# Kernel tuning notes

Hardware: AMD Instinct MI355X
Metric: run time of the kernel (lower is better)

Reference implementation:

```python
import jax, jax.numpy as jnp
import numpy as np

B, L, C, H, W = 4, 16, 64, 64, 64
F, NH, NB = 128, 2, 2


def _ln(x, w, b, eps=1e-5):
    # LayerNorm over last two dims (H, W), torch-style biased variance
    m = jnp.mean(x, axis=(-2, -1), keepdims=True)
    v = jnp.var(x, axis=(-2, -1), keepdims=True)
    return (x - m) * jax.lax.rsqrt(v + eps) * w + b


def _conv2d(x, w, b):
    # x: (N, Cin, H, W), w: (Cout, Cin, k, k) -- the (1,k,k) Conv3d acts per-frame
    y = jax.lax.conv_general_dilated(x, w, (1, 1), 'SAME',
                                     dimension_numbers=('NCHW', 'OIHW', 'NCHW'))
    return y + b[None, :, None, None]


def _combine(c1, c2):
    a1, b1 = c1
    a2, b2 = c2
    return a1 * a2, a2 * b1 + b2


def _forward(x, params_log, pBw_r, pBw_i, pBb_r, pBb_i, pCw_r, pCw_i, pCb_r, pCb_i,
             lru_ln_w, lru_ln_b, cin_w, cin_b, h3_w, h3_b, h1_w, h1_b,
             h_ln_w, h_ln_b, cout_w, cout_b, ffn_ln_w, ffn_ln_b):
    gelu = lambda t: jax.nn.gelu(t, approximate=False)
    Bsz, Ln, Cc, Hh, Ww = x.shape
    for i in range(NB):
        # ---- ConvLRULayer ----
        pl = params_log[i]
        nu = jnp.exp(pl[:Cc])            # (C, H)
        theta = jnp.exp(pl[Cc:2 * Cc])   # (C, H)
        gamma = jnp.exp(pl[2 * Cc:])     # (C, H)
        lamb = jnp.exp(jax.lax.complex(-nu, theta))  # (C, H) complex
        Bw = jax.lax.complex(pBw_r[i], pBw_i[i])
        Bb = jax.lax.complex(pBb_r[i], pBb_i[i])
        Cw = jax.lax.complex(pCw_r[i], pCw_i[i])
        Cb = jax.lax.complex(pCb_r[i], pCb_i[i])
        h = jnp.fft.fft2(x.astype(jnp.complex64), axes=(-2, -1))  # (B,L,C,H,W)
        h = jnp.einsum('blchw,oc->blohw', h, Bw) + Bb[None, None, :, None, None]
        h = h * gamma[None, None, :, :, None]
        # parallel scan: h[t] = lamb * h[t-1] + h[t] along L
        a = jnp.broadcast_to(lamb[None, None, :, :, None], (Bsz, Ln, Cc, Hh, 1))
        _, h = jax.lax.associative_scan(_combine, (a, h), axis=1)
        h = jnp.fft.ifft2(h, axes=(-2, -1))
        h = jnp.einsum('blchw,oc->blohw', h, Cw) + Cb[None, None, :, None, None]
        h = _ln(h.real, lru_ln_w[i], lru_ln_b[i])
        x = h + x
        # ---- FeedForward (all Conv3d have kernel 1 in L -> per-frame 2D) ----
        y = x.reshape(Bsz * Ln, Cc, Hh, Ww)
        y_ = gelu(_conv2d(y, cin_w[i], cin_b[i]))  # (B*L, F, H, W)
        for j in range(NH):
            t = gelu(_conv2d(y_, h3_w[i, j], h3_b[i, j]))
            t = gelu(jnp.einsum('nfhw,of->nohw', t, h1_w[i, j])
                     + h1_b[i, j][None, :, None, None])
            y_ = _ln(t, h_ln_w[i, j], h_ln_b[i, j]) + y_
        t = jnp.einsum('nfhw,of->nohw', y_, cout_w[i]) + cout_b[i][None, :, None, None]
        t = _ln(t, ffn_ln_w[i], ffn_ln_b[i])
        x = t.reshape(Bsz, Ln, Cc, Hh, Ww) + x
    return x


def setup_inputs() -> dict:
    key = jax.random.key(0)
    ks = jax.random.split(key, 16)
    x = jax.random.normal(ks[0], (B, L, C, H, W), jnp.float32)
    # LRU stability init (as in the torch module)
    r_min, r_max = 0.8, 0.99
    u1 = jax.random.uniform(ks[1], (NB, C, H), jnp.float32)
    u2 = jax.random.uniform(ks[2], (NB, C, H), jnp.float32)
    nu_log = jnp.log(-0.5 * jnp.log(u1 * (r_max ** 2 - r_min ** 2) + r_min ** 2))
    theta_log = jnp.log(u2 * 2.0 * np.pi)
    gamma_log = 0.5 * jnp.log(1.0 - jnp.exp(-2.0 * jnp.exp(nu_log)))
    params_log = jnp.concatenate([nu_log, theta_log, gamma_log], axis=1)  # (NB, 3C, H)

    def nrm(k, shape, fan_in):
        return jax.random.normal(k, shape, jnp.float32) / np.sqrt(fan_in)

    return dict(
        x=x, params_log=params_log,
        pBw_r=nrm(ks[3], (NB, C, C), C), pBw_i=jnp.zeros((NB, C, C), jnp.float32),
        pBb_r=jnp.zeros((NB, C), jnp.float32), pBb_i=jnp.zeros((NB, C), jnp.float32),
        pCw_r=nrm(ks[4], (NB, C, C), C), pCw_i=jnp.zeros((NB, C, C), jnp.float32),
        pCb_r=jnp.zeros((NB, C), jnp.float32), pCb_i=jnp.zeros((NB, C), jnp.float32),
        lru_ln_w=jnp.ones((NB, H, W), jnp.float32), lru_ln_b=jnp.zeros((NB, H, W), jnp.float32),
        cin_w=nrm(ks[5], (NB, F, C, 7, 7), C * 49), cin_b=jnp.zeros((NB, F), jnp.float32),
        h3_w=nrm(ks[6], (NB, NH, F, F, 3, 3), F * 9), h3_b=jnp.zeros((NB, NH, F), jnp.float32),
        h1_w=nrm(ks[7], (NB, NH, F, F), F), h1_b=jnp.zeros((NB, NH, F), jnp.float32),
        h_ln_w=jnp.ones((NB, NH, H, W), jnp.float32), h_ln_b=jnp.zeros((NB, NH, H, W), jnp.float32),
        cout_w=nrm(ks[8], (NB, C, F), F), cout_b=jnp.zeros((NB, C), jnp.float32),
        ffn_ln_w=jnp.ones((NB, H, W), jnp.float32), ffn_ln_b=jnp.zeros((NB, H, W), jnp.float32),
    )


def reference(x, params_log, pBw_r, pBw_i, pBb_r, pBb_i, pCw_r, pCw_i, pCb_r, pCb_i,
              lru_ln_w, lru_ln_b, cin_w, cin_b, h3_w, h3_b, h1_w, h1_b,
              h_ln_w, h_ln_b, cout_w, cout_b, ffn_ln_w, ffn_ln_b):
    return _forward(x, params_log, pBw_r, pBw_i, pBb_r, pBb_i, pCw_r, pCw_i,
                    pCb_r, pCb_i, lru_ln_w, lru_ln_b, cin_w, cin_b, h3_w, h3_b,
                    h1_w, h1_b, h_ln_w, h_ln_b, cout_w, cout_b, ffn_ln_w, ffn_ln_b)
```

## Files before the change

kernel.cpp:

```cpp
#include <hip/hip_runtime.h>
#include <math.h>

static constexpr int Bd = 4, Ld = 16, Cd = 64, Hd = 64, Wd = 64, Fd = 128;
static constexpr int NBLK = 2, NHEAD = 2;
static constexpr int HW = 4096;
static constexpr float TWO_PI = 6.28318530717958647692f;

typedef __attribute__((ext_vector_type(8))) short bf16x8;
typedef __attribute__((ext_vector_type(4))) float f32x4;
typedef __attribute__((ext_vector_type(4))) unsigned int u32x4;

__device__ __forceinline__ float gelu_f(float v) {
    return 0.5f * v * (1.f + erff(v * 0.7071067811865476f));
}

__device__ __forceinline__ unsigned short bf16c(float f) {
    unsigned int u = __float_as_uint(f);
    unsigned int r = (u + 0x7fffu + ((u >> 16) & 1u)) >> 16;
    return (unsigned short)r;
}
__device__ __forceinline__ float bf2f(unsigned short u) {
    return __uint_as_float((unsigned int)u << 16);
}
__device__ __forceinline__ unsigned int packbf(float r, float i) {
    return (unsigned int)bf16c(r) | ((unsigned int)bf16c(i) << 16);
}
__device__ __forceinline__ bf16x8 bneg(bf16x8 v) {
    u32x4 u = *(u32x4*)&v;
    u = u ^ 0x80008000u;
    return *(bf16x8*)&u;
}

__device__ __forceinline__ void gl2lds16(const void* g, void* l) {
    __builtin_amdgcn_global_load_lds(
        (const __attribute__((address_space(1))) void*)g,
        (__attribute__((address_space(3))) void*)l, 16, 0, 0);
}

__global__ void k_prepdft(unsigned short* __restrict__ o) {
    int idx = blockIdx.x * 256 + threadIdx.x;
    if (idx >= 16384) return;
    int sec = idx >> 12, j = idx & 4095;
    int a = j >> 6, b = j & 63;
    float ang = (TWO_PI / 64.f) * (float)((a * b) & 63);
    float sv, cv;
    __sincosf(ang, &sv, &cv);
    float v;
    if (sec == 0) v = cv;
    else if (sec == 1) v = -sv;
    else if (sec == 2) v = cv * (1.f / 64.f);
    else v = -sv * (1.f / 64.f);
    o[idx] = bf16c(v);
}

__global__ void k_preplru(const float* __restrict__ bwr, const float* __restrict__ bwi,
                          const float* __restrict__ cwr, const float* __restrict__ cwi,
                          const float* __restrict__ gl,
                          unsigned short* __restrict__ wout, float* __restrict__ gamT) {
    int idx = blockIdx.x * 256 + threadIdx.x;
    if (idx < 16384) {
        int sec = idx >> 12, j = idx & 4095;
        const float* s = (sec == 0) ? bwr : (sec == 1) ? bwi : (sec == 2) ? cwr : cwi;
        wout[idx] = bf16c(s[j]);
    } else if (idx < 20480) {
        int j = idx - 16384;
        int fh = j >> 6, o2 = j & 63;
        gamT[j] = __expf(gl[o2 * 64 + fh]);
    }
}

__global__ __launch_bounds__(256) void k_dfthm(const float* __restrict__ x,
                                               unsigned int* __restrict__ X,
                                               const unsigned short* __restrict__ tcb,
                                               const unsigned short* __restrict__ tsb) {
    __shared__ __align__(16) unsigned char smm[49152];
    unsigned char* xpT = smm;
    unsigned char* tC = smm + 32768;
    unsigned char* tS = smm + 40960;
    int blk = blockIdx.x;
    int fi = blk >> 4;
    int w0 = (blk & 15) * 4;
    int t = threadIdx.x, lane = t & 63, wv = t >> 6;
    int pl = lane & 15, kg = lane >> 4;
    int l3 = lane >> 3, l7 = lane & 7;

    for (int q = 0; q < 2; ++q) {
        int sg = q * 4 + wv;
        gl2lds16(tcb + (size_t)(sg * 8 + l3) * 64 + (l7 ^ l3) * 8, tC + sg * 1024);
        gl2lds16(tsb + (size_t)(sg * 8 + l3) * 64 + (l7 ^ l3) * 8, tS + sg * 1024);
    }
    const float* xf = x + (size_t)fi * Cd * HW;
    int h = t & 63;
    for (int k = 0; k < 16; ++k) {
        int c = k * 4 + (t >> 6);
        float4 v = *(const float4*)(xf + (size_t)c * HW + h * 64 + w0);
        float vv[4] = {v.x, v.y, v.z, v.w};
#pragma unroll
        for (int q = 0; q < 4; ++q) {
            int pos = q * 64 + c;
            *(unsigned short*)(xpT + pos * 128 + ((h * 2) ^ ((c & 7) << 4))) = bf16c(vv[q]);
        }
    }
    __syncthreads();

    int w = w0 + wv;
    unsigned int* Xw = X + (size_t)fi * 262144 + (size_t)w * 4096;
    for (int half = 0; half < 2; ++half) {
        f32x4 aR[2][4], aI[2][4];
#pragma unroll
        for (int mt = 0; mt < 2; ++mt)
#pragma unroll
            for (int nt = 0; nt < 4; ++nt) { aR[mt][nt] = (f32x4)0.f; aI[mt][nt] = (f32x4)0.f; }
#pragma unroll
        for (int ks = 0; ks < 2; ++ks) {
            int koff = (ks * 64 + kg * 16);
            bf16x8 ac[2], as_[2], b[4];
#pragma unroll
            for (int mt = 0; mt < 2; ++mt) {
                int row = half * 32 + mt * 16 + pl;
                int off = row * 128 + (koff ^ ((pl & 7) << 4));
                ac[mt] = *(const bf16x8*)(tC + off);
                as_[mt] = *(const bf16x8*)(tS + off);
            }
#pragma unroll
            for (int nt = 0; nt < 4; ++nt) {
                int pos = wv * 64 + nt * 16 + pl;
                b[nt] = *(const bf16x8*)(xpT + pos * 128 + (koff ^ ((pl & 7) << 4)));
            }
#pragma unroll
            for (int mt = 0; mt < 2; ++mt)
#pragma unroll
                for (int nt = 0; nt < 4; ++nt) {
                    aR[mt][nt] = __builtin_amdgcn_mfma_f32_16x16x32_bf16(ac[mt], b[nt], aR[mt][nt], 0, 0, 0);
                    aI[mt][nt] = __builtin_amdgcn_mfma_f32_16x16x32_bf16(as_[mt], b[nt], aI[mt][nt], 0, 0, 0);
                }
        }
#pragma unroll
        for (int mt = 0; mt < 2; ++mt)
#pragma unroll
            for (int nt = 0; nt < 4; ++nt) {
                int c = nt * 16 + pl;
#pragma unroll
                for (int r = 0; r < 4; ++r) {
                    int fh = half * 32 + mt * 16 + kg * 4 + r;
                    Xw[fh * 64 + c] = packbf(aR[mt][nt][r], aI[mt][nt][r]);
                }
            }
    }
}

__global__ __launch_bounds__(256) void k_lrumid(unsigned int* __restrict__ X,
                                                const unsigned short* __restrict__ wbr,
                                                const unsigned short* __restrict__ wbi,
                                                const unsigned short* __restrict__ wcr,
                                                const unsigned short* __restrict__ wci,
                                                const float* __restrict__ gamT,
                                                const float* __restrict__ br_g,
                                                const float* __restrict__ bi_g,
                                                const float* __restrict__ plg) {
    __shared__ __align__(16) unsigned char smm[81920];
    unsigned char* inr = smm;
    unsigned char* ini = smm + 8192;
    unsigned char* hre = smm + 16384;
    unsigned char* him = smm + 24576;
    unsigned char* wBR = smm + 32768;
    unsigned char* wBI = smm + 40960;
    unsigned char* wCR = smm + 49152;
    unsigned char* wCI = smm + 57344;
    float* gam = (float*)(smm + 65536);
    int blk = blockIdx.x;
    int b = blk >> 6, s = blk & 63;
    int t = threadIdx.x, lane = t & 63, wv = t >> 6;
    int pj = lane & 15, kg = lane >> 4;
    int l3 = lane >> 3, l7 = lane & 7;

    for (int q = 0; q < 2; ++q) {
        int sg = q * 4 + wv;
        size_t goff = (size_t)(sg * 8 + l3) * 64 + (l7 ^ l3) * 8;
        gl2lds16(wbr + goff, wBR + sg * 1024);
        gl2lds16(wbi + goff, wBI + sg * 1024);
        gl2lds16(wcr + goff, wCR + sg * 1024);
        gl2lds16(wci + goff, wCI + sg * 1024);
    }
    for (int j = t; j < 4096; j += 256) gam[j] = gamT[j];

    float lamr[4][4], lami[4][4];
#pragma unroll
    for (int nt = 0; nt < 4; ++nt) {
        int o = nt * 16 + pj;
#pragma unroll
        for (int r = 0; r < 4; ++r) {
            int fh = wv * 16 + kg * 4 + r;
            float nu = expf(plg[o * 64 + fh]);
            float th = expf(plg[4096 + o * 64 + fh]);
            float mag = expf(-nu);
            float sth, cth;
            sincosf(th, &sth, &cth);
            lamr[nt][r] = mag * cth;
            lami[nt][r] = mag * sth;
        }
    }
    float bRo[4], bIo[4];
#pragma unroll
    for (int nt = 0; nt < 4; ++nt) {
        bRo[nt] = (s == 0) ? br_g[nt * 16 + pj] : 0.f;
        bIo[nt] = (s == 0) ? bi_g[nt * 16 + pj] : 0.f;
    }
    float str[4][4], sti[4][4];
    unsigned int* Xfrm = X + (size_t)b * 16 * 262144 + (size_t)s * 4096;

    for (int l = 0; l < 16; ++l) {
        unsigned int* Xi = Xfrm + (size_t)l * 262144;
        __syncthreads();
        for (int k = 0; k < 4; ++k) {
            int j = k * 256 + t;
            int row = j >> 4, c0 = (j & 15) * 4;
            u32x4 v = *(const u32x4*)(Xi + (size_t)row * 64 + c0);
            unsigned int rw0 = (v.x & 0xffffu) | (v.y << 16);
            unsigned int rw1 = (v.z & 0xffffu) | (v.w << 16);
            unsigned int iw0 = (v.x >> 16) | (v.y & 0xffff0000u);
            unsigned int iw1 = (v.z >> 16) | (v.w & 0xffff0000u);
            int off = row * 128 + ((((c0 >> 3) ^ (row & 7)) << 4) | ((c0 & 7) * 2));
            *(unsigned int*)(inr + off) = rw0;
            *(unsigned int*)(inr + off + 4) = rw1;
            *(unsigned int*)(ini + off) = iw0;
            *(unsigned int*)(ini + off + 4) = iw1;
        }
        __syncthreads();

        f32x4 cR[4], cI[4];
#pragma unroll
        for (int nt = 0; nt < 4; ++nt) { cR[nt] = (f32x4)0.f; cI[nt] = (f32x4)0.f; }
#pragma unroll
        for (int ks = 0; ks < 2; ++ks) {
            int koff = ks * 64 + kg * 16;
            int aoff = (wv * 16 + pj) * 128 + (koff ^ ((pj & 7) << 4));
            bf16x8 ar = *(const bf16x8*)(inr + aoff);
            bf16x8 ai = *(const bf16x8*)(ini + aoff);
            bf16x8 an = bneg(ai);
#pragma unroll
            for (int nt = 0; nt < 4; ++nt) {
                int o = nt * 16 + pj;
                int woff = o * 128 + (koff ^ ((pj & 7) << 4));
                bf16x8 brf = *(const bf16x8*)(wBR + woff);
                bf16x8 bif = *(const bf16x8*)(wBI + woff);
                cR[nt] = __builtin_amdgcn_mfma_f32_16x16x32_bf16(ar, brf, cR[nt], 0, 0, 0);
                cR[nt] = __builtin_amdgcn_mfma_f32_16x16x32_bf16(an, bif, cR[nt], 0, 0, 0);
                cI[nt] = __builtin_amdgcn_mfma_f32_16x16x32_bf16(ar, bif, cI[nt], 0, 0, 0);
                cI[nt] = __builtin_amdgcn_mfma_f32_16x16x32_bf16(ai, brf, cI[nt], 0, 0, 0);
            }
        }
#pragma unroll
        for (int nt = 0; nt < 4; ++nt) {
            int o = nt * 16 + pj;
#pragma unroll
            for (int r = 0; r < 4; ++r) {
                int row = wv * 16 + kg * 4 + r;
                float g = gam[row * 64 + o];
                float vr = (cR[nt][r] + bRo[nt]) * g;
                float vi = (cI[nt][r] + bIo[nt]) * g;
                if (l == 0) {
                    str[nt][r] = vr;
                    sti[nt][r] = vi;
                } else {
                    float nr = lamr[nt][r] * str[nt][r] - lami[nt][r] * sti[nt][r] + vr;
                    float ni = lamr[nt][r] * sti[nt][r] + lami[nt][r] * str[nt][r] + vi;
                    str[nt][r] = nr;
                    sti[nt][r] = ni;
                }
                int hoff = row * 128 + ((((o >> 3) ^ (row & 7)) << 4) | ((o & 7) * 2));
                *(unsigned short*)(hre + hoff) = bf16c(str[nt][r]);
                *(unsigned short*)(him + hoff) = bf16c(sti[nt][r]);
            }
        }
        __syncthreads();

        f32x4 dR[4], dI[4];
#pragma unroll
        for (int nt = 0; nt < 4; ++nt) { dR[nt] = (f32x4)0.f; dI[nt] = (f32x4)0.f; }
#pragma unroll
        for (int ks = 0; ks < 2; ++ks) {
            int koff = ks * 64 + kg * 16;
            int aoff = (wv * 16 + pj) * 128 + (koff ^ ((pj & 7) << 4));
            bf16x8 ar = *(const bf16x8*)(hre + aoff);
            bf16x8 ai = *(const bf16x8*)(him + aoff);
            bf16x8 an = bneg(ai);
#pragma unroll
            for (int nt = 0; nt < 4; ++nt) {
                int o = nt * 16 + pj;
                int woff = o * 128 + (koff ^ ((pj & 7) << 4));
                bf16x8 brf = *(const bf16x8*)(wCR + woff);
                bf16x8 bif = *(const bf16x8*)(wCI + woff);
                dR[nt] = __builtin_amdgcn_mfma_f32_16x16x32_bf16(ar, brf, dR[nt], 0, 0, 0);
                dR[nt] = __builtin_amdgcn_mfma_f32_16x16x32_bf16(an, bif, dR[nt], 0, 0, 0);
                dI[nt] = __builtin_amdgcn_mfma_f32_16x16x32_bf16(ar, bif, dI[nt], 0, 0, 0);
                dI[nt] = __builtin_amdgcn_mfma_f32_16x16x32_bf16(ai, brf, dI[nt], 0, 0, 0);
            }
        }
#pragma unroll
        for (int nt = 0; nt < 4; ++nt) {
            int o = nt * 16 + pj;
#pragma unroll
            for (int r = 0; r < 4; ++r) {
                int row = wv * 16 + kg * 4 + r;
                Xi[(size_t)row * 64 + o] = packbf(dR[nt][r], dI[nt][r]);
            }
        }
    }
}

__global__ __launch_bounds__(256) void k_idfthm_ln(const unsigned int* __restrict__ X,
                                                   const unsigned short* __restrict__ tic,
                                                   const unsigned short* __restrict__ tis,
                                                   const float* __restrict__ cbr,
                                                   const float* __restrict__ lnw,
                                                   const float* __restrict__ lnb,
                                                   const float* __restrict__ xprev,
                                                   float* __restrict__ xout) {
    __shared__ __align__(16) unsigned char smm[81920];
    unsigned char* SrT = smm;
    unsigned char* SiT = smm + 32768;
    unsigned char* tC = smm + 65536;
    unsigned char* tS = smm + 73728;
    float* y4 = (float*)smm;
    int blk = blockIdx.x;
    int fi = blk >> 4;
    int c0 = (blk & 15) * 4;
    int t = threadIdx.x, lane = t & 63, wv = t >> 6;
    int pl = lane & 15, kg = lane >> 4;
    int l3 = lane >> 3, l7 = lane & 7;

    for (int q = 0; q < 2; ++q) {
        int sg = q * 4 + wv;
        gl2lds16(tic + (size_t)(sg * 8 + l3) * 64 + (l7 ^ l3) * 8, tC + sg * 1024);
        gl2lds16(tis + (size_t)(sg * 8 + l3) * 64 + (l7 ^ l3) * 8, tS + sg * 1024);
    }
    const unsigned int* Xf = X + (size_t)fi * 262144;
    int fh = t & 63;
    for (int k = 0; k < 16; ++k) {
        int w = k * 4 + (t >> 6);
        u32x4 v = *(const u32x4*)(Xf + (size_t)w * 4096 + fh * 64 + c0);
        unsigned int vv[4] = {v.x, v.y, v.z, v.w};
#pragma unroll
        for (int cj = 0; cj < 4; ++cj) {
            int pos2 = w * 4 + cj;
            int off = pos2 * 128 + ((fh * 2) ^ ((pos2 & 7) << 4));
            *(unsigned short*)(SrT + off) = (unsigned short)(vv[cj] & 0xffffu);
            *(unsigned short*)(SiT + off) = (unsigned short)(vv[cj] >> 16);
        }
    }
    __syncthreads();

    f32x4 y[4][4];
#pragma unroll
    for (int mt = 0; mt < 4; ++mt)
#pragma unroll
        for (int nt = 0; nt < 4; ++nt) y[mt][nt] = (f32x4)0.f;
#pragma unroll
    for (int ks = 0; ks < 2; ++ks) {
        int koff = ks * 64 + kg * 16;
        bf16x8 ac[4], as_[4], brf[4], bif[4];
#pragma unroll
        for (int mt = 0; mt < 4; ++mt) {
            int row = mt * 16 + pl;
            int off = row * 128 + (koff ^ ((pl & 7) << 4));
            ac[mt] = *(const bf16x8*)(tC + off);
            as_[mt] = *(const bf16x8*)(tS + off);
        }
#pragma unroll
        for (int nt = 0; nt < 4; ++nt) {
            int pos2 = wv * 64 + nt * 16 + pl;
            int off = pos2 * 128 + (koff ^ ((pl & 7) << 4));
            brf[nt] = *(const bf16x8*)(SrT + off);
            bif[nt] = *(const bf16x8*)(SiT + off);
        }
#pragma unroll
        for (int mt = 0; mt < 4; ++mt)
#pragma unroll
            for (int nt = 0; nt < 4; ++nt) {
                y[mt][nt] = __builtin_amdgcn_mfma_f32_16x16x32_bf16(ac[mt], brf[nt], y[mt][nt], 0, 0, 0);
                y[mt][nt] = __builtin_amdgcn_mfma_f32_16x16x32_bf16(as_[mt], bif[nt], y[mt][nt], 0, 0, 0);
            }
    }
    __syncthreads();

    float cb4[4];
#pragma unroll
    for (int cj = 0; cj < 4; ++cj) cb4[cj] = cbr[c0 + cj];
#pragma unroll
    for (int mt = 0; mt < 4; ++mt)
#pragma unroll
        for (int nt = 0; nt < 4; ++nt) {
            int pos2 = wv * 64 + nt * 16 + pl;
            int w = pos2 >> 2, cj = pos2 & 3;
#pragma unroll
            for (int r = 0; r < 4; ++r) {
                int h = mt * 16 + kg * 4 + r;
                y4[cj * 4232 + h * 66 + w] = y[mt][nt][r] + cb4[cj];
            }
        }
    __syncthreads();

    int w = lane;
    const float* yp = y4 + wv * 4232;
    float s = 0.f, q = 0.f;
    for (int h = 0; h < 64; ++h) {
        float v = yp[h * 66 + w];
        s += v;
        q += v * v;
    }
#pragma unroll
    for (int off = 32; off; off >>= 1) {
        s += __shfl_xor(s, off);
        q += __shfl_xor(q, off);
    }
    float m = s * (1.f / 4096.f);
    float var = q * (1.f / 4096.f) - m * m;
    float rs = rsqrtf(var + 1e-5f);
    int c = c0 + wv;
    const float* xp = xprev + ((size_t)fi * Cd + c) * HW;
    float* xo = xout + ((size_t)fi * Cd + c) * HW;
    for (int h = 0; h < 64; ++h) {
        int p = h * 64 + w;
        xo[p] = (yp[h * 66 + w] - m) * rs * lnw[p] + lnb[p] + xp[p];
    }
}

__global__ __launch_bounds__(256) void k_ln_res(const unsigned short* __restrict__ t_in,
                                                const float* __restrict__ w,
                                                const float* __restrict__ b,
                                                float* __restrict__ dst) {
    __shared__ float red[8];
    int fr = blockIdx.x;
    int t = threadIdx.x;
    const unsigned short* src = t_in + (size_t)fr * HW + t * 16;
    float* d = dst + (size_t)fr * HW + t * 16;
    u32x4 v0 = *(const u32x4*)(src);
    u32x4 v1 = *(const u32x4*)(src + 8);
    float vals[16];
    unsigned int vw[8] = {v0.x, v0.y, v0.z, v0.w, v1.x, v1.y, v1.z, v1.w};
#pragma unroll
    for (int j = 0; j < 8; ++j) {
        vals[j * 2] = bf2f((unsigned short)(vw[j] & 0xffffu));
        vals[j * 2 + 1] = bf2f((unsigned short)(vw[j] >> 16));
    }
    float s = 0.f, sq = 0.f;
#pragma unroll
    for (int j = 0; j < 16; ++j) { s += vals[j]; sq += vals[j] * vals[j]; }
    for (int off = 32; off; off >>= 1) {
        s += __shfl_down(s, off);
        sq += __shfl_down(sq, off);
    }
    int wid = t >> 6;
    if ((t & 63) == 0) { red[wid] = s; red[4 + wid] = sq; }
    __syncthreads();
    s = red[0] + red[1] + red[2] + red[3];
    sq = red[4] + red[5] + red[6] + red[7];
    float m = s * (1.f / 4096.f);
    float var = sq * (1.f / 4096.f) - m * m;
    float rs = rsqrtf(var + 1e-5f);
    const float* wp = w + t * 16;
    const float* bp = b + t * 16;
#pragma unroll
    for (int q4 = 0; q4 < 4; ++q4) {
        float4 wv4 = *(const float4*)(wp + q4 * 4);
        float4 bv4 = *(const float4*)(bp + q4 * 4);
        float4 dv = *(const float4*)(d + q4 * 4);
        dv.x += (vals[q4 * 4 + 0] - m) * rs * wv4.x + bv4.x;
        dv.y += (vals[q4 * 4 + 1] - m) * rs * wv4.y + bv4.y;
        dv.z += (vals[q4 * 4 + 2] - m) * rs * wv4.z + bv4.z;
        dv.w += (vals[q4 * 4 + 3] - m) * rs * wv4.w + bv4.w;
        *(float4*)(d + q4 * 4) = dv;
    }
}

__global__ void k_prep7(const float* __restrict__ w, unsigned short* __restrict__ o) {
    int idx = blockIdx.x * 256 + threadIdx.x;
    if (idx < 49 * 128 * 64) {
        int tap = idx >> 13, rem = idx & 8191, f = rem >> 6, c = rem & 63;
        o[idx] = bf16c(w[(size_t)(f * 64 + c) * 49 + tap]);
    }
}
__global__ void k_prep3(const float* __restrict__ w, unsigned short* __restrict__ o,
                        int nh) {
    int idx = blockIdx.x * 256 + threadIdx.x;
    if (idx < nh * 147456) {
        int head = idx / 147456;
        int rem = idx - head * 147456;
        int tap = rem >> 14, r2 = rem & 16383, f = r2 >> 7, c = r2 & 127;
        o[idx] = bf16c(w[(size_t)head * 147456 + (size_t)(f * 128 + c) * 9 + tap]);
    }
}
__global__ void k_prepcvt(const float* __restrict__ w, unsigned short* __restrict__ o, int n) {
    int idx = blockIdx.x * 256 + threadIdx.x;
    if (idx < n) o[idx] = bf16c(w[idx]);
}

__global__ __launch_bounds__(256) void k_t2p(const float* __restrict__ x,
                                             unsigned short* __restrict__ xT) {
    __shared__ float tile[64][65];
    int blk = blockIdx.x;
    int f = blk >> 6;
    int p0 = (blk & 63) * 64;
    int t = threadIdx.x;
    const float* src = x + (size_t)f * Cd * HW;
    for (int j = t; j < 4096; j += 256) {
        int c = j >> 6, p = j & 63;
        tile[c][p] = src[(size_t)c * HW + p0 + p];
    }
    __syncthreads();
    unsigned short* dst = xT + ((size_t)f * HW + p0) * 64;
    for (int j = t; j < 4096; j += 256) {
        int p = j >> 6, c = j & 63;
        dst[(size_t)p * 64 + c] = bf16c(tile[c][p]);
    }
}

__global__ __launch_bounds__(512) void k_conv7m(const unsigned short* __restrict__ xT,
                                                const unsigned short* __restrict__ wb,
                                                const float* __restrict__ bias,
                                                unsigned short* __restrict__ yout) {
    __shared__ __align__(16) unsigned char smm[158208];
    unsigned char* inT = smm;
    unsigned char* wt0 = smm + 125440;
    int blk = blockIdx.x;
    int fi = blk >> 3;
    int y0 = (blk & 7) * 8;
    int t = threadIdx.x, lane = t & 63, wv = t >> 6;
    int l3 = lane >> 3, l7 = lane & 7;

    const unsigned short* xf = xT + (size_t)fi * HW * 64;
    float4 z4 = make_float4(0.f, 0.f, 0.f, 0.f);
    int ksw_in = l7 ^ ((3 + l3) & 7);
    for (int idx = wv; idx < 112; idx += 8) {
        int r = idx >> 3, sg = idx & 7;
        int srow = y0 + r - 3;
        unsigned char* dst = inT + r * 8960 + 3 * 128 + sg * 1024;
        if (srow >= 0 && srow < 64) {
            gl2lds16(xf + (size_t)srow * 4096 + (sg * 8 + l3) * 64 + ksw_in * 8, dst);
        } else {
            *(float4*)(dst + lane * 16) = z4;
        }
    }
    for (int j = t; j < 672; j += 512) {
        int r = j / 48, k = j % 48;
        int xp = (k < 24) ? (k >> 3) : 67 + ((k - 24) >> 3);
        *(float4*)(inT + r * 8960 + xp * 128 + (k & 7) * 16) = z4;
    }
    int ksw_w = l7 ^ l3;
    for (int q = 0; q < 2; ++q) {
        int sg = q * 8 + wv;
        int f = sg * 8 + l3;
        gl2lds16(wb + (size_t)f * 64 + ksw_w * 8, wt0 + sg * 1024);
    }
    __syncthreads();

    int wm = wv & 3, wn = wv >> 2;
    f32x4 acc[8][4];
#pragma unroll
    for (int m = 0; m < 8; ++m)
#pragma unroll
        for (int n = 0; n < 4; ++n) acc[m][n] = (f32x4)0.f;
    int kg = lane >> 4, pl = lane & 15;
    int cur = 0;
    for (int tap = 0; tap < 49; ++tap) {
        if (tap + 1 < 49) {
            const unsigned short* g = wb + (size_t)(tap + 1) * 8192;
            unsigned char* wdst = wt0 + (cur ^ 1) * 16384;
            for (int q = 0; q < 2; ++q) {
                int sg = q * 8 + wv;
                int f = sg * 8 + l3;
                gl2lds16(g + (size_t)f * 64 + ksw_w * 8, wdst + sg * 1024);
            }
        }
        unsigned char* wcur = wt0 + cur * 16384;
        int ky = tap / 7, kx = tap % 7;
#pragma unroll
        for (int ks = 0; ks < 2; ++ks) {
            bf16x8 a[8], b[4];
#pragma unroll
            for (int m = 0; m < 8; ++m) {
                int row = wm * 2 + (m >> 2) + ky;
                int xp = (m & 3) * 16 + pl + kx;
                a[m] = *(const bf16x8*)(inT + row * 8960 + xp * 128 +
                                        (((ks * 4 + kg) ^ (xp & 7)) << 4));
            }
#pragma unroll
            for (int n = 0; n < 4; ++n) {
                int rowf = wn * 64 + n * 16 + pl;
                b[n] = *(const bf16x8*)(wcur + rowf * 128 +
                                        (((ks * 4 + kg) ^ (pl & 7)) << 4));
            }
#pragma unroll
            for (int m = 0; m < 8; ++m)
#pragma unroll
                for (int n = 0; n < 4; ++n)
                    acc[m][n] = __builtin_amdgcn_mfma_f32_16x16x32_bf16(a[m], b[n], acc[m][n], 0, 0, 0);
        }
        __syncthreads();
        cur ^= 1;
    }
    unsigned short* yo = yout + ((size_t)fi * HW + (size_t)y0 * 64) * 128;
#pragma unroll
    for (int m = 0; m < 8; ++m) {
        int rowl = wm * 2 + (m >> 2);
#pragma unroll
        for (int n = 0; n < 4; ++n) {
            int f = wn * 64 + n * 16 + pl;
            float bs = bias[f];
#pragma unroll
            for (int r = 0; r < 4; ++r) {
                int x = (m & 3) * 16 + kg * 4 + r;
                yo[(size_t)(rowl * 64 + x) * 128 + f] = bf16c(gelu_f(acc[m][n][r] + bs));
            }
        }
    }
}

__global__ __launch_bounds__(512) void k_conv3f(const unsigned short* __restrict__ yin,
                                                const unsigned short* __restrict__ wb,
                                                const float* __restrict__ bias3,
                                                const unsigned short* __restrict__ w1,
                                                const float* __restrict__ bias1,
                                                unsigned short* __restrict__ outp2,
                                                float* __restrict__ lnpart) {
    __shared__ __align__(16) unsigned char smm[134144];
    __shared__ float redS[8][64], redQ[8][64];
    unsigned char* inT = smm;
    unsigned char* wL = smm + 101376;
    int blk = blockIdx.x;
    int fi = blk >> 4;
    int y0 = (blk & 15) * 4;
    int t = threadIdx.x, lane = t & 63, wv = t >> 6;
    int l4 = lane >> 4, l15 = lane & 15;
    const unsigned short* yf = yin + (size_t)fi * HW * 128;
    float4 z4 = make_float4(0.f, 0.f, 0.f, 0.f);
    for (int seg = wv; seg < 96; seg += 8) {
        int r = seg >> 4, xs = seg & 15;
        int srow = y0 + r - 1;
        int xp = 1 + xs * 4 + l4;
        unsigned char* dst = inT + r * 16896 + (size_t)(1 + xs * 4) * 256;
        if (srow >= 0 && srow < 64) {
            int gsrc = l15 ^ (xp & 7);
            gl2lds16(yf + ((size_t)(srow * 64 + xp - 1) * 128 + gsrc * 8), dst);
        } else {
            *(float4*)(dst + lane * 16) = z4;
        }
    }
    if (t < 192) {
        int r = t / 32, k = t & 31;
        int xp = (k < 16) ? 0 : 65;
        *(float4*)(inT + r * 16896 + xp * 256 + (k & 15) * 16) = z4;
    }
    for (int sg = wv; sg < 32; sg += 8) {
        int f = sg * 4 + l4;
        gl2lds16(wb + (size_t)f * 128 + (l15 ^ (f & 7)) * 8, wL + sg * 1024);
    }
    __syncthreads();

    int wm = wv & 3, wn = wv >> 2;
    f32x4 acc[4][4];
#pragma unroll
    for (int m = 0; m < 4; ++m)
#pragma unroll
        for (int n = 0; n < 4; ++n) acc[m][n] = (f32x4)0.f;
    int kg = lane >> 4, pl = lane & 15;
    int fw = t >> 2, qw = t & 3;
    u32x4 rg[4];
    for (int tap = 0; tap < 9; ++tap) {
        if (tap < 8) {
            const u32x4* src = (const u32x4*)(wb + (size_t)(tap + 1) * 16384 +
                                              (size_t)fw * 128 + qw * 32);
#pragma unroll
            for (int j = 0; j < 4; ++j) rg[j] = src[j];
        }
        int ky = tap / 3, kx = tap % 3;
        int rbase = (wm + ky) * 16896;
#pragma unroll
        for (int ks = 0; ks < 4; ++ks) {
            bf16x8 a[4], b[4];
#pragma unroll
            for (int m = 0; m < 4; ++m) {
                int xp = m * 16 + pl + kx;
                a[m] = *(const bf16x8*)(inT + rbase + (size_t)xp * 256 +
                                        ((ks * 64 + kg * 16) ^ ((xp & 7) << 4)));
            }
#pragma unroll
            for (int n = 0; n < 4; ++n) {
                int row = wn * 64 + n * 16 + pl;
                b[n] = *(const bf16x8*)(wL + (size_t)row * 256 +
                                        ((ks * 64 + kg * 16) ^ ((pl & 7) << 4)));
            }
#pragma unroll
            for (int m = 0; m < 4; ++m)
#pragma unroll
                for (int n = 0; n < 4; ++n)
                    acc[m][n] = __builtin_amdgcn_mfma_f32_16x16x32_bf16(a[m], b[n], acc[m][n], 0, 0, 0);
        }
        __syncthreads();
        if (tap < 8) {
#pragma unroll
            for (int j = 0; j < 4; ++j)
                *(u32x4*)(wL + (size_t)fw * 256 + (((qw * 4 + j) ^ (fw & 7)) << 4)) = rg[j];
        }
        __syncthreads();
    }

    unsigned char* tL = smm;
    unsigned char* w1L = smm + 65536;
#pragma unroll
    for (int m = 0; m < 4; ++m)
#pragma unroll
        for (int n = 0; n < 4; ++n) {
            int f = wn * 64 + n * 16 + pl;
            float bs = bias3[f];
#pragma unroll
            for (int r = 0; r < 4; ++r) {
                int pos = wm * 64 + m * 16 + kg * 4 + r;
                *(unsigned short*)(tL + (size_t)pos * 256 +
                    ((((f >> 3) ^ (pos & 7)) << 4) | ((f & 7) * 2))) =
                    bf16c(gelu_f(acc[m][n][r] + bs));
            }
        }
    for (int sg = wv; sg < 32; sg += 8) {
        int rr = sg * 4 + l4;
        gl2lds16(w1 + (size_t)rr * 128 + (l15 ^ (rr & 7)) * 8, w1L + sg * 1024);
    }
    __syncthreads();

    f32x4 fa[4][4];
#pragma unroll
    for (int m = 0; m < 4; ++m)
#pragma unroll
        for (int n = 0; n < 4; ++n) fa[m][n] = (f32x4)0.f;
#pragma unroll
    for (int ks = 0; ks < 4; ++ks) {
        bf16x8 a[4], b[4];
#pragma unroll
        for (int m = 0; m < 4; ++m) {
            int row = wm * 64 + m * 16 + pl;
            a[m] = *(const bf16x8*)(tL + (size_t)row * 256 +
                                    ((ks * 64 + kg * 16) ^ ((pl & 7) << 4)));
        }
#pragma unroll
        for (int n = 0; n < 4; ++n) {
            int row = wn * 64 + n * 16 + pl;
            b[n] = *(const bf16x8*)(w1L + (size_t)row * 256 +
                                    ((ks * 64 + kg * 16) ^ ((pl & 7) << 4)));
        }
#pragma unroll
        for (int m = 0; m < 4; ++m)
#pragma unroll
            for (int n = 0; n < 4; ++n)
                fa[m][n] = __builtin_amdgcn_mfma_f32_16x16x32_bf16(a[m], b[n], fa[m][n], 0, 0, 0);
    }
    __syncthreads();

    int slab = blk & 15;
    int p0 = slab * 256;
    unsigned char* oL = smm;
#pragma unroll
    for (int n = 0; n < 4; ++n) {
        int f = wn * 64 + n * 16 + pl;
        float bs = bias1[f];
        float s = 0.f, q = 0.f;
#pragma unroll
        for (int m = 0; m < 4; ++m)
#pragma unroll
            for (int r = 0; r < 4; ++r) {
                float v = gelu_f(fa[m][n][r] + bs);
                int pos = wm * 64 + m * 16 + kg * 4 + r;
                *(unsigned short*)(oL + (size_t)pos * 256 +
                    ((((f >> 3) ^ (pos & 7)) << 4) | ((f & 7) * 2))) = bf16c(v);
                s += v;
                q += v * v;
            }
        s += __shfl_xor(s, 16); s += __shfl_xor(s, 32);
        q += __shfl_xor(q, 16); q += __shfl_xor(q, 32);
        if (kg == 0) { redS[wv][n * 16 + pl] = s; redQ[wv][n * 16 + pl] = q; }
    }
    __syncthreads();
    unsigned char* o0 = (unsigned char*)(outp2 + ((size_t)fi * HW + p0) * 128);
#pragma unroll
    for (int it = 0; it < 8; ++it) {
        int gid = it * 512 + t;
        int pos = gid >> 4, g = gid & 15;
        u32x4 v = *(const u32x4*)(oL + (size_t)pos * 256 + ((g ^ (pos & 7)) << 4));
        *(u32x4*)(o0 + (size_t)pos * 256 + g * 16) = v;
    }
    if (t < 128) {
        int wh = t >> 6, j = t & 63;
        float s = redS[wh * 4][j] + redS[wh * 4 + 1][j] + redS[wh * 4 + 2][j] + redS[wh * 4 + 3][j];
        float q = redQ[wh * 4][j] + redQ[wh * 4 + 1][j] + redQ[wh * 4 + 2][j] + redQ[wh * 4 + 3][j];
        float* lp = lnpart + ((size_t)(fi * 16 + slab) * 128 + t) * 2;
        lp[0] = s;
        lp[1] = q;
    }
}

__global__ __launch_bounds__(256) void k_lnapply2(const unsigned short* __restrict__ t2,
                                                  const float* __restrict__ lnpart,
                                                  const float* __restrict__ w,
                                                  const float* __restrict__ b,
                                                  unsigned short* __restrict__ y) {
    __shared__ float sm_m[128], sm_r[128];
    int blk = blockIdx.x;
    int fi = blk >> 5, p0 = (blk & 31) * 128;
    int t = threadIdx.x;
    if (t < 128) {
        float s = 0.f, q = 0.f;
        for (int sl = 0; sl < 16; ++sl) {
            const float* lp = lnpart + ((size_t)(fi * 16 + sl) * 128 + t) * 2;
            s += lp[0];
            q += lp[1];
        }
        float m = s * (1.f / 4096.f);
        float var = q * (1.f / 4096.f) - m * m;
        sm_m[t] = m;
        sm_r[t] = rsqrtf(var + 1e-5f);
    }
    __syncthreads();
    int f = t & 127, ph = t >> 7;
    for (int k = ph; k < 128; k += 2) {
        int p = p0 + k;
        size_t idx = ((size_t)fi * HW + p) * 128 + f;
        float v = bf2f(t2[idx]);
        float yv = bf2f(y[idx]);
        y[idx] = bf16c(yv + (v - sm_m[f]) * sm_r[f] * w[p] + b[p]);
    }
}

__global__ __launch_bounds__(256) void k_coutm(const unsigned short* __restrict__ yin,
                                               const unsigned short* __restrict__ wt,
                                               const float* __restrict__ bias,
                                               unsigned short* __restrict__ outp) {
    __shared__ __align__(16) unsigned char smm[49152];
    unsigned char* inL = smm;
    unsigned char* wL = smm + 32768;
    int blk = blockIdx.x;
    int fi = blk >> 5;
    int p0 = (blk & 31) * 128;
    int t = threadIdx.x, lane = t & 63, wv = t >> 6;
    int l4 = lane >> 4, l15 = lane & 15;
    for (int sg = wv; sg < 16; sg += 4) {
        int r = sg * 4 + l4;
        gl2lds16(wt + (size_t)r * 128 + (l15 ^ (r & 7)) * 8, wL + sg * 1024);
    }
    const unsigned short* yb = yin + (size_t)fi * HW * 128;
    for (int sg = wv; sg < 32; sg += 4) {
        int pos = sg * 4 + l4;
        gl2lds16(yb + ((size_t)(p0 + pos) * 128 + (l15 ^ (pos & 7)) * 8), inL + sg * 1024);
    }
    __syncthreads();
    int wm = wv & 1, wn = wv >> 1;
    f32x4 acc[2][4];
#pragma unroll
    for (int m = 0; m < 2; ++m)
#pragma unroll
        for (int n = 0; n < 4; ++n) acc[m][n] = (f32x4)0.f;
    int kg = lane >> 4, pl = lane & 15;
#pragma unroll
    for (int ks = 0; ks < 4; ++ks) {
        bf16x8 a[2], b[4];
#pragma unroll
        for (int m = 0; m < 2; ++m) {
            int row = wm * 32 + m * 16 + pl;
            a[m] = *(const bf16x8*)(wL + (size_t)row * 256 +
                                    ((ks * 64 + kg * 16) ^ ((pl & 7) << 4)));
        }
#pragma unroll
        for (int n = 0; n < 4; ++n) {
            int row = wn * 64 + n * 16 + pl;
            b[n] = *(const bf16x8*)(inL + (size_t)row * 256 +
                                    ((ks * 64 + kg * 16) ^ ((pl & 7) << 4)));
        }
#pragma unroll
        for (int m = 0; m < 2; ++m)
#pragma unroll
            for (int n = 0; n < 4; ++n)
                acc[m][n] = __builtin_amdgcn_mfma_f32_16x16x32_bf16(a[m], b[n], acc[m][n], 0, 0, 0);
    }
    __syncthreads();
    unsigned char* oL = smm;
#pragma unroll
    for (int m = 0; m < 2; ++m)
#pragma unroll
        for (int n = 0; n < 4; ++n) {
            int posl = wn * 64 + n * 16 + pl;
#pragma unroll
            for (int r = 0; r < 4; ++r) {
                int c = wm * 32 + m * 16 + kg * 4 + r;
                *(unsigned short*)(oL + (size_t)c * 256 +
                    ((((posl >> 3) ^ (c & 7)) << 4) | ((posl & 7) * 2))) =
                    bf16c(acc[m][n][r] + bias[c]);
            }
        }
    __syncthreads();
#pragma unroll
    for (int it = 0; it < 4; ++it) {
        int gid = it * 256 + t;
        int c = gid >> 4, g = gid & 15;
        u32x4 v = *(const u32x4*)(oL + (size_t)c * 256 + ((g ^ (c & 7)) << 4));
        *(u32x4*)((unsigned char*)(outp + ((size_t)fi * 64 + c) * HW + p0) + g * 16) = v;
    }
}

extern "C" void kernel_launch(void* const* d_in, const int* in_sizes, int n_in,
                              void* d_out, int out_size, void* d_ws, size_t ws_size,
                              hipStream_t stream) {
    (void)in_sizes; (void)n_in; (void)out_size;
    const float* x_in  = (const float*)d_in[0];
    const float* pl    = (const float*)d_in[1];
    const float* pBw_r = (const float*)d_in[2];
    const float* pBw_i = (const float*)d_in[3];
    const float* pBb_r = (const float*)d_in[4];
    const float* pBb_i = (const float*)d_in[5];
    const float* pCw_r = (const float*)d_in[6];
    const float* pCw_i = (const float*)d_in[7];
    const float* pCb_r = (const float*)d_in[8];
    const float* pCb_i = (const float*)d_in[9];
    const float* lruw  = (const float*)d_in[10];
    const float* lrub  = (const float*)d_in[11];
    const float* cinw  = (const float*)d_in[12];
    const float* cinb  = (const float*)d_in[13];
    const float* h3w   = (const float*)d_in[14];
    const float* h3b   = (const float*)d_in[15];
    const float* h1w   = (const float*)d_in[16];
    const float* h1b   = (const float*)d_in[17];
    const float* hlnw  = (const float*)d_in[18];
    const float* hlnb  = (const float*)d_in[19];
    const float* coutw = (const float*)d_in[20];
    const float* coutb = (const float*)d_in[21];
    const float* flnw  = (const float*)d_in[22];
    const float* flnb  = (const float*)d_in[23];
    float* out = (float*)d_out;

    int FR = 8, LB = 1;
    {
        const int frs[6] = {64, 32, 16, 16, 8, 8};
        const int lbs[6] = {4, 4, 4, 2, 2, 1};
        for (int k = 0; k < 6; ++k) {
            size_t region = (size_t)lbs[k] * 16777216ULL;
            size_t ffn = (size_t)frs[k] * 3145728ULL;
            if (ffn > region) region = ffn;
            size_t needb = region + 1605632ULL + (size_t)frs[k] * 32768ULL + 65536ULL;
            if (needb <= ws_size) { FR = frs[k]; LB = lbs[k]; break; }
        }
    }
    size_t region = (size_t)LB * 16777216ULL;
    {
        size_t ffn = (size_t)FR * 3145728ULL;
        if (ffn > region) region = ffn;
    }
    unsigned char* ws = (unsigned char*)d_ws;
    unsigned int* Xb = (unsigned int*)ws;
    unsigned short* ybuf = (unsigned short*)ws;
    unsigned short* t2bf = (unsigned short*)(ws + (size_t)FR * 1048576);
    unsigned short* xT   = (unsigned short*)(ws + (size_t)FR * 2097152);
    unsigned short* cobuf = (unsigned short*)(ws + (size_t)FR * 2621440);
    unsigned char* wbase = ws + region;
    unsigned short* wb7  = (unsigned short*)(wbase);
    unsigned short* wb3  = (unsigned short*)(wbase + 802816);
    unsigned short* wb1  = (unsigned short*)(wbase + 1392640);
    unsigned short* wbco = (unsigned short*)(wbase + 1458176);
    unsigned short* dftT = (unsigned short*)(wbase + 1474560);
    unsigned short* lruW = (unsigned short*)(wbase + 1507328);
    float* gamT          = (float*)(wbase + 1540096);
    float* lnpart        = (float*)(wbase + 1556480);
    unsigned short* tcb = dftT;
    unsigned short* tsb = dftT + 4096;
    unsigned short* tic = dftT + 8192;
    unsigned short* tis = dftT + 12288;
    unsigned short* wBr = lruW;
    unsigned short* wBi = lruW + 4096;
    unsigned short* wCr = lruW + 8192;
    unsigned short* wCi = lruW + 12288;

    const int NCl = 4 / LB;
    const int NCf = 64 / FR;

    k_prepdft<<<64, 256, 0, stream>>>(dftT);

    for (int i = 0; i < NBLK; ++i) {
        const float* xsrc = (i == 0) ? x_in : out;

        k_preplru<<<80, 256, 0, stream>>>(pBw_r + (size_t)i * 4096,
                                          pBw_i + (size_t)i * 4096,
                                          pCw_r + (size_t)i * 4096,
                                          pCw_i + (size_t)i * 4096,
                                          pl + (size_t)i * 12288 + 8192, lruW, gamT);
        for (int cc = 0; cc < NCl; ++cc) {
            size_t boff = (size_t)cc * LB * 4194304;
            k_dfthm<<<LB * 256, 256, 0, stream>>>(xsrc + boff, Xb, tcb, tsb);
            k_lrumid<<<LB * 64, 256, 0, stream>>>(Xb, wBr, wBi, wCr, wCi, gamT,
                                                  pBb_r + (size_t)i * 64,
                                                  pBb_i + (size_t)i * 64,
                                                  pl + (size_t)i * 12288);
            k_idfthm_ln<<<LB * 256, 256, 0, stream>>>(Xb, tic, tis,
                                                      pCb_r + (size_t)i * 64,
                                                      lruw + (size_t)i * 4096,
                                                      lrub + (size_t)i * 4096,
                                                      xsrc + boff, out + boff);
        }

        k_prep7<<<1568, 256, 0, stream>>>(cinw + (size_t)i * 401408, wb7);
        k_prep3<<<1152, 256, 0, stream>>>(h3w + (size_t)i * 2 * 147456, wb3, 2);
        k_prepcvt<<<128, 256, 0, stream>>>(h1w + (size_t)i * 2 * 16384, wb1, 32768);
        k_prepcvt<<<32, 256, 0, stream>>>(coutw + (size_t)i * 8192, wbco, 8192);

        for (int cc = 0; cc < NCf; ++cc) {
            float* xb = out + (size_t)cc * FR * 262144;
            k_t2p<<<FR * 64, 256, 0, stream>>>(xb, xT);
            k_conv7m<<<FR * 8, 512, 0, stream>>>(xT, wb7, cinb + (size_t)i * 128, ybuf);
            for (int j = 0; j < NHEAD; ++j) {
                k_conv3f<<<FR * 16, 512, 0, stream>>>(ybuf, wb3 + (size_t)j * 147456,
                                                      h3b + (size_t)(i * 2 + j) * 128,
                                                      wb1 + (size_t)j * 16384,
                                                      h1b + (size_t)(i * 2 + j) * 128,
                                                      t2bf, lnpart);
                k_lnapply2<<<FR * 32, 256, 0, stream>>>(t2bf, lnpart,
                                                        hlnw + (size_t)(i * 2 + j) * 4096,
                                                        hlnb + (size_t)(i * 2 + j) * 4096,
                                                        ybuf);
            }
            k_coutm<<<FR * 32, 256, 0, stream>>>(ybuf, wbco, coutb + (size_t)i * 64, cobuf);
            k_ln_res<<<FR * 64, 256, 0, stream>>>(cobuf, flnw + (size_t)i * 4096,
                                                  flnb + (size_t)i * 4096, xb);
        }
    }
}
```

Before: 1.856 ms.

## Halve conv3 LDS footprint by splitting channels into two passes for 2-block occupancy

The fused 3x3+1x1 conv kernel now processes its 128 input channels in two halves of 64. The input tile and weight tile in LDS are each half as large, which cuts shared memory from about 134KB to 67KB and allows launch_bounds(512,2) so two blocks can fit per CU. The 1x1 weights are read straight from global memory instead of being staged in LDS. In exchange, the tiles are loaded twice, there are twice as many tap loops and barriers, the 1x1 B-operand loads are uncoalesced global reads, and the register cap may cause spills.

```diff
diff --git a/kernel.cpp b/kernel.cpp
--- a/kernel.cpp
+++ b/kernel.cpp
@@ -617,97 +617,100 @@
     }
 }
 
-__global__ __launch_bounds__(512) void k_conv3f(const unsigned short* __restrict__ yin,
-                                                const unsigned short* __restrict__ wb,
-                                                const float* __restrict__ bias3,
-                                                const unsigned short* __restrict__ w1,
-                                                const float* __restrict__ bias1,
-                                                unsigned short* __restrict__ outp2,
-                                                float* __restrict__ lnpart) {
-    __shared__ __align__(16) unsigned char smm[134144];
+__global__ __launch_bounds__(512, 2) void k_conv3f(const unsigned short* __restrict__ yin,
+                                                   const unsigned short* __restrict__ wb,
+                                                   const float* __restrict__ bias3,
+                                                   const unsigned short* __restrict__ w1,
+                                                   const float* __restrict__ bias1,
+                                                   unsigned short* __restrict__ outp2,
+                                                   float* __restrict__ lnpart) {
+    __shared__ __align__(16) unsigned char smm[67072];
     __shared__ float redS[8][64], redQ[8][64];
     unsigned char* inT = smm;
-    unsigned char* wL = smm + 101376;
+    unsigned char* wL = smm + 50688;
     int blk = blockIdx.x;
     int fi = blk >> 4;
     int y0 = (blk & 15) * 4;
     int t = threadIdx.x, lane = t & 63, wv = t >> 6;
-    int l4 = lane >> 4, l15 = lane & 15;
+    int l3 = lane >> 3, l7 = lane & 7;
+    int kg = lane >> 4, pl = lane & 15;
+    int wm = wv & 3, wn = wv >> 2;
     const unsigned short* yf = yin + (size_t)fi * HW * 128;
     float4 z4 = make_float4(0.f, 0.f, 0.f, 0.f);
-    for (int seg = wv; seg < 96; seg += 8) {
-        int r = seg >> 4, xs = seg & 15;
-        int srow = y0 + r - 1;
-        int xp = 1 + xs * 4 + l4;
-        unsigned char* dst = inT + r * 16896 + (size_t)(1 + xs * 4) * 256;
-        if (srow >= 0 && srow < 64) {
-            int gsrc = l15 ^ (xp & 7);
-            gl2lds16(yf + ((size_t)(srow * 64 + xp - 1) * 128 + gsrc * 8), dst);
-        } else {
-            *(float4*)(dst + lane * 16) = z4;
-        }
-    }
-    if (t < 192) {
-        int r = t / 32, k = t & 31;
-        int xp = (k < 16) ? 0 : 65;
-        *(float4*)(inT + r * 16896 + xp * 256 + (k & 15) * 16) = z4;
-    }
-    for (int sg = wv; sg < 32; sg += 8) {
-        int f = sg * 4 + l4;
-        gl2lds16(wb + (size_t)f * 128 + (l15 ^ (f & 7)) * 8, wL + sg * 1024);
-    }
-    __syncthreads();
-
-    int wm = wv & 3, wn = wv >> 2;
+
     f32x4 acc[4][4];
 #pragma unroll
     for (int m = 0; m < 4; ++m)
 #pragma unroll
         for (int n = 0; n < 4; ++n) acc[m][n] = (f32x4)0.f;
-    int kg = lane >> 4, pl = lane & 15;
+
     int fw = t >> 2, qw = t & 3;
-    u32x4 rg[4];
-    for (int tap = 0; tap < 9; ++tap) {
-        if (tap < 8) {
-            const u32x4* src = (const u32x4*)(wb + (size_t)(tap + 1) * 16384 +
-                                              (size_t)fw * 128 + qw * 32);
-#pragma unroll
-            for (int j = 0; j < 4; ++j) rg[j] = src[j];
-        }
-        int ky = tap / 3, kx = tap % 3;
-        int rbase = (wm + ky) * 16896;
-#pragma unroll
-        for (int ks = 0; ks < 4; ++ks) {
-            bf16x8 a[4], b[4];
-#pragma unroll
-            for (int m = 0; m < 4; ++m) {
-                int xp = m * 16 + pl + kx;
-                a[m] = *(const bf16x8*)(inT + rbase + (size_t)xp * 256 +
-                                        ((ks * 64 + kg * 16) ^ ((xp & 7) << 4)));
-            }
-#pragma unroll
-            for (int n = 0; n < 4; ++n) {
-                int row = wn * 64 + n * 16 + pl;
-                b[n] = *(const bf16x8*)(wL + (size_t)row * 256 +
-                                        ((ks * 64 + kg * 16) ^ ((pl & 7) << 4)));
-            }
-#pragma unroll
-            for (int m = 0; m < 4; ++m)
-#pragma unroll
-                for (int n = 0; n < 4; ++n)
-                    acc[m][n] = __builtin_amdgcn_mfma_f32_16x16x32_bf16(a[m], b[n], acc[m][n], 0, 0, 0);
+    for (int kp = 0; kp < 2; ++kp) {
+        for (int seg = wv; seg < 48; seg += 8) {
+            int r = seg >> 3, xg = seg & 7;
+            int srow = y0 + r - 1;
+            int xp = 1 + xg * 8 + l3;
+            unsigned char* dst = inT + r * 8448 + (size_t)(1 + xg * 8) * 128;
+            if (srow >= 0 && srow < 64) {
+                int gs = l7 ^ (xp & 7);
+                gl2lds16(yf + ((size_t)(srow * 64 + xp - 1) * 128 + kp * 64 + gs * 8), dst);
+            } else {
+                *(float4*)(dst + lane * 16) = z4;
+            }
+        }
+        if (t < 96) {
+            int r = t >> 4, k = t & 15;
+            int xp = (k < 8) ? 0 : 65;
+            *(float4*)(inT + r * 8448 + xp * 128 + (k & 7) * 16) = z4;
+        }
+        for (int sg = wv; sg < 16; sg += 8) {
+            int f = sg * 8 + l3;
+            gl2lds16(wb + (size_t)f * 128 + kp * 64 + (l7 ^ l3) * 8, wL + sg * 1024);
         }
         __syncthreads();
-        if (tap < 8) {
-#pragma unroll
-            for (int j = 0; j < 4; ++j)
-                *(u32x4*)(wL + (size_t)fw * 256 + (((qw * 4 + j) ^ (fw & 7)) << 4)) = rg[j];
-        }
-        __syncthreads();
+
+        u32x4 rg[2];
+        for (int tap = 0; tap < 9; ++tap) {
+            if (tap < 8) {
+                const unsigned short* src = wb + (size_t)(tap + 1) * 16384 +
+                                            (size_t)fw * 128 + kp * 64;
+#pragma unroll
+                for (int j = 0; j < 2; ++j) rg[j] = ((const u32x4*)src)[qw * 2 + j];
+            }
+            int ky = tap / 3, kx = tap % 3;
+            int rbase = (wm + ky) * 8448;
+#pragma unroll
+            for (int ks = 0; ks < 2; ++ks) {
+                bf16x8 a[4], b[4];
+#pragma unroll
+                for (int m = 0; m < 4; ++m) {
+                    int xp = m * 16 + pl + kx;
+                    a[m] = *(const bf16x8*)(inT + rbase + xp * 128 +
+                                            (((ks * 4 + kg) ^ (xp & 7)) << 4));
+                }
+#pragma unroll
+                for (int n = 0; n < 4; ++n) {
+                    int f = wn * 64 + n * 16 + pl;
+                    b[n] = *(const bf16x8*)(wL + f * 128 +
+                                            (((ks * 4 + kg) ^ (f & 7)) << 4));
+                }
+#pragma unroll
+                for (int m = 0; m < 4; ++m)
+#pragma unroll
+                    for (int n = 0; n < 4; ++n)
+                        acc[m][n] = __builtin_amdgcn_mfma_f32_16x16x32_bf16(a[m], b[n], acc[m][n], 0, 0, 0);
+            }
+            __syncthreads();
+            if (tap < 8) {
+#pragma unroll
+                for (int j = 0; j < 2; ++j)
+                    *(u32x4*)(wL + fw * 128 + (((qw * 2 + j) ^ (fw & 7)) << 4)) = rg[j];
+            }
+            __syncthreads();
+        }
     }
 
     unsigned char* tL = smm;
-    unsigned char* w1L = smm + 65536;
 #pragma unroll
     for (int m = 0; m < 4; ++m)
 #pragma unroll
@@ -722,10 +725,6 @@
                     bf16c(gelu_f(acc[m][n][r] + bs));
             }
         }
-    for (int sg = wv; sg < 32; sg += 8) {
-        int rr = sg * 4 + l4;
-        gl2lds16(w1 + (size_t)rr * 128 + (l15 ^ (rr & 7)) * 8, w1L + sg * 1024);
-    }
     __syncthreads();
 
     f32x4 fa[4][4];
@@ -736,16 +735,15 @@
 #pragma unroll
     for (int ks = 0; ks < 4; ++ks) {
         bf16x8 a[4], b[4];
+#pragma unroll
+        for (int n = 0; n < 4; ++n) {
+            int o = wn * 64 + n * 16 + pl;
+            b[n] = *(const bf16x8*)(w1 + (size_t)o * 128 + ks * 32 + kg * 8);
+        }
 #pragma unroll
         for (int m = 0; m < 4; ++m) {
             int row = wm * 64 + m * 16 + pl;
             a[m] = *(const bf16x8*)(tL + (size_t)row * 256 +
-                                    ((ks * 64 + kg * 16) ^ ((pl & 7) << 4)));
-        }
-#pragma unroll
-        for (int n = 0; n < 4; ++n) {
-            int row = wn * 64 + n * 16 + pl;
-            b[n] = *(const bf16x8*)(w1L + (size_t)row * 256 +
                                     ((ks * 64 + kg * 16) ^ ((pl & 7) << 4)));
         }
 #pragma unroll
```

Result: no change. 1.892 ms (+2.0%).
